# Performance work log

Measured on AMD Instinct MI355X. Metric: run time of the kernel, lower is better.

The kernel has to match this reference:

```python
import jax, jax.numpy as jnp
import numpy as np

RADII = (0.4, 0.8, 1.2)
SIGMA2 = 2.0 * 0.2 ** 2   # Gaussian shell-density bandwidth
ALPHA = 0.3               # keras LeakyReLU default
EPS = 1e-3                # keras BatchNormalization default epsilon


def _n_coeffs(L):
    return sum((2 * l + 1) ** 2 for l in range(L + 1))


def _pullback_idx(L):
    # flat index of Wigner block entry (m, n=0) for each SH coeff (l, m)
    idx, off = [], 0
    for l in range(L + 1):
        d = 2 * l + 1
        idx += [off + m * d + l for m in range(d)]
        off += d * d
    return np.asarray(idx, dtype=np.int32)


def setup_inputs() -> dict:
    key = jax.random.key(0)
    ks = jax.random.split(key, 20)
    B, N, Q, S = 64, 2048, 1024, 512
    T = [_n_coeffs(l) for l in (5, 4, 3)]  # 286, 165, 84
    f32 = jnp.float32

    def nrm(k, shape, scale=1.0):
        return jax.random.normal(ks[k], shape, dtype=f32) * scale

    dirs = nrm(1, (3, S, 3))
    dirs = dirs / jnp.linalg.norm(dirs, axis=-1, keepdims=True)
    z = lambda n: jnp.zeros((n,), f32)
    o = lambda n: jnp.ones((n,), f32)
    return {
        "x": nrm(0, (B, N, 3)),
        "shell_dirs": dirs,                                   # [3, 512, 3]
        "A_sh": nrm(2, (36, S), 1.0 / np.sqrt(S)),            # SH projection (l_max=5)
        "D_eval0": nrm(3, (Q, T[0]), 1.0 / np.sqrt(T[0])),    # Wigner eval bases
        "D_eval1": nrm(4, (Q, T[1]), 1.0 / np.sqrt(T[1])),
        "D_eval2": nrm(5, (Q, T[2]), 1.0 / np.sqrt(T[2])),
        "D_coef1": nrm(6, (T[1], Q), 1.0 / np.sqrt(Q)),       # Wigner coeff (projection) bases
        "D_coef2": nrm(7, (T[2], Q), 1.0 / np.sqrt(Q)),
        "D_coef_last": nrm(8, (T[2], Q), 1.0 / np.sqrt(Q)),
        "W0": nrm(9, (3, 16), 1.0 / np.sqrt(3)), "b0": z(16),
        "W1": nrm(10, (16, 32), 0.25), "b1": z(32),
        "W2": nrm(11, (32, 64), 1.0 / np.sqrt(32)), "b2": z(64),
        "g0": o(16), "be0": z(16),
        "g1": o(32), "be1": z(32),
        "g2": o(64), "be2": z(64),
        "Wfc1": nrm(12, (256, 512), 1.0 / 16.0), "bfc1": z(512),
        "gfc1": o(512), "befc1": z(512),
        "Wfc2": nrm(13, (512, 256), 1.0 / np.sqrt(512)), "bfc2": z(256),
        "gfc2": o(256), "befc2": z(256),
        "Wout": nrm(14, (256, 40), 1.0 / 16.0), "bout": z(40),
    }


def _bn(y, g, b, axes):
    m = jnp.mean(y, axis=axes, keepdims=True)
    v = jnp.var(y, axis=axes, keepdims=True)
    return (y - m) * jax.lax.rsqrt(v + EPS) * g + b


def reference(x, shell_dirs, A_sh, D_eval0, D_eval1, D_eval2,
              D_coef1, D_coef2, D_coef_last,
              W0, b0, W1, b1, W2, b2,
              g0, be0, g1, be1, g2, be2,
              Wfc1, bfc1, gfc1, befc1, Wfc2, bfc2, gfc2, befc2,
              Wout, bout):
    B = x.shape[0]
    # --- sphere_shell_embedding: Gaussian shell density -> SH coeffs per shell ---
    xn2 = jnp.sum(x * x, -1)[..., None]                 # [B,N,1]
    sh = []
    for i, r in enumerate(RADII):
        c = r * shell_dirs[i]                           # [S,3]
        d2 = xn2 + jnp.sum(c * c, -1) - 2.0 * (x @ c.T)  # [B,N,S]
        f = jnp.mean(jnp.exp(-d2 / SIGMA2), axis=1)      # [B,S]
        sh.append(f @ A_sh.T)                            # [B,36]
    sh = jnp.stack(sh, axis=-1)                          # [B,36,3] shells as channels
    # --- S2_to_SO3_pullback: Y_lm -> D^l_{m,0} column of Wigner blocks ---
    idx = jnp.asarray(_pullback_idx(5))
    y = jnp.zeros((B, 286, 3), sh.dtype).at[:, idx, :].set(sh)
    # --- layer 0: SO3Conv (per-coeff channel mix) + WignerEval + BN + LReLU + WignerCoeffs ---
    y = jnp.einsum('btc,cu->btu', y, W0) + b0
    y = jnp.einsum('qt,btu->bqu', D_eval0, y)            # [B,1024,16]
    y = jax.nn.leaky_relu(_bn(y, g0, be0, (0, 1)), ALPHA)
    y = jnp.einsum('tq,bqu->btu', D_coef1, y)            # [B,165,16]
    # --- layer 1 ---
    y = jnp.einsum('btc,cu->btu', y, W1) + b1
    y = jnp.einsum('qt,btu->bqu', D_eval1, y)            # [B,1024,32]
    y = jax.nn.leaky_relu(_bn(y, g1, be1, (0, 1)), ALPHA)
    y = jnp.einsum('tq,bqu->btu', D_coef2, y)            # [B,84,32]
    # --- layer 2 ---
    y = jnp.einsum('btc,cu->btu', y, W2) + b2
    y = jnp.einsum('qt,btu->bqu', D_eval2, y)            # [B,1024,64]
    y = jax.nn.leaky_relu(_bn(y, g2, be2, (0, 1)), ALPHA)
    y = jnp.einsum('tq,bqu->btu', D_coef_last, y)        # [B,84,64]
    # --- degree-wise norms (rotation-invariant pooling), l_max=3 blocks ---
    offs, sizes = (0, 1, 10, 35), (1, 9, 25, 49)
    feats = jnp.concatenate(
        [jnp.linalg.norm(y[:, o:o + s, :], axis=1, keepdims=True)
         for o, s in zip(offs, sizes)], axis=1)          # [B,4,64]
    h = feats.reshape(B, -1)                             # [B,256]
    # --- MLP head (dropout = identity at inference) ---
    h = jax.nn.relu(_bn(h @ Wfc1 + bfc1, gfc1, befc1, (0,)))
    h = jax.nn.relu(_bn(h @ Wfc2 + bfc2, gfc2, befc2, (0,)))
    return jax.nn.softmax(h @ Wout + bout, axis=-1)
```

## Files before the change

### kernel.cpp

```cpp
#include <hip/hip_runtime.h>
#include <hip/hip_bf16.h>

#define BB 64
#define NN 2048
#define QQ 1024
#define SS 512
#define NCH 16
#define PREPB 609
#define QKN3 8

__device__ const int PIDX[36] = {
    0, 2, 5, 8, 12, 17, 22, 27, 32, 38, 45, 52, 59, 66, 73, 80,
    88, 97, 106, 115, 124, 133, 142, 151, 160,
    170, 181, 192, 203, 214, 225, 236, 247, 258, 269, 280};

__global__ __launch_bounds__(256) void k_preshell(
    const float* __restrict__ De0, const float* __restrict__ De1, const float* __restrict__ De2,
    float* __restrict__ Dg0t, float* __restrict__ rs0,
    float* __restrict__ Det1, float* __restrict__ Det2,
    float* __restrict__ stats,
    const float* __restrict__ x, const float* __restrict__ dirs, float* __restrict__ pbuf) {
    __shared__ float tile[32][33];
    __shared__ float4 lx[NN / NCH];
    int blk = blockIdx.x, tid = threadIdx.x;
    if (blk < PREPB) {
        int r = tid >> 5, c = tid & 31;
        if (blk < 192) {
            int tq = blk & 31, tt = blk >> 5;
            int q0 = tq * 32, t0 = tt * 32;
            for (int rr = r; rr < 32; rr += 8) {
                int t = t0 + c;
                tile[rr][c] = (t < 165) ? De1[(q0 + rr) * 165 + t] : 0.f;
            }
            __syncthreads();
            for (int rr = r; rr < 32; rr += 8) {
                int t = t0 + rr;
                if (t < 165) Det1[t * QQ + q0 + c] = tile[c][rr];
            }
        } else if (blk < 288) {
            int i = blk - 192;
            int tq = i & 31, tt = i >> 5;
            int q0 = tq * 32, t0 = tt * 32;
            for (int rr = r; rr < 32; rr += 8) {
                int t = t0 + c;
                tile[rr][c] = (t < 84) ? De2[(q0 + rr) * 84 + t] : 0.f;
            }
            __syncthreads();
            for (int rr = r; rr < 32; rr += 8) {
                int t = t0 + rr;
                if (t < 84) Det2[t * QQ + q0 + c] = tile[c][rr];
            }
        } else if (blk < 352) {
            int i = blk - 288;
            int tq = i & 31, tj = i >> 5;
            int q0 = tq * 32, j0 = tj * 32;
            for (int rr = r; rr < 32; rr += 8) {
                int j = j0 + c;
                tile[rr][c] = (j < 36) ? De0[(q0 + rr) * 286 + PIDX[j]] : 0.f;
            }
            __syncthreads();
            for (int rr = r; rr < 32; rr += 8) {
                int j = j0 + rr;
                if (j < 36) Dg0t[j * QQ + q0 + c] = tile[c][rr];
            }
        } else if (blk < 608) {
            int w = tid >> 6, lane = tid & 63;
            int q = (blk - 352) * 4 + w;
            float s = 0.f;
#pragma unroll
            for (int p = 0; p < 5; p++) {
                int idx = lane + p * 64;
                if (idx < 286) s += De0[q * 286 + idx];
            }
#pragma unroll
            for (int o = 32; o > 0; o >>= 1) s += __shfl_xor(s, o, 64);
            if (lane == 0) rs0[q] = s;
        } else {
            if (tid < 224) stats[tid] = 0.f;
        }
        return;
    }
    int idx = blk - PREPB;
    int b = idx & 63, zc = idx >> 6;
    const float KL = 18.033688011112042f;
    const float* xb = x + ((size_t)b * NN + zc * (NN / NCH)) * 3;
    for (int n = tid; n < NN / NCH; n += 256) {
        float X = xb[n * 3 + 0];
        float Y = xb[n * 3 + 1];
        float Z = xb[n * 3 + 2];
        lx[n] = make_float4(X, Y, Z, -KL * (X * X + Y * Y + Z * Z));
    }
    __syncthreads();
    float cxs[3][2], cys[3][2], czs[3][2], bas[3][2];
#pragma unroll
    for (int i = 0; i < 3; i++) {
        float r = (i == 0) ? 0.4f : ((i == 1) ? 0.8f : 1.2f);
#pragma unroll
        for (int h = 0; h < 2; h++) {
            int s = tid + h * 256;
            float cx = r * dirs[(i * SS + s) * 3 + 0];
            float cy = r * dirs[(i * SS + s) * 3 + 1];
            float cz = r * dirs[(i * SS + s) * 3 + 2];
            bas[i][h] = -KL * (cx * cx + cy * cy + cz * cz);
            cxs[i][h] = 2.f * KL * cx;
            cys[i][h] = 2.f * KL * cy;
            czs[i][h] = 2.f * KL * cz;
        }
    }
    float acc[3][2];
#pragma unroll
    for (int i = 0; i < 3; i++) { acc[i][0] = 0.f; acc[i][1] = 0.f; }
#pragma unroll 4
    for (int n = 0; n < NN / NCH; n++) {
        float4 p = lx[n];
#pragma unroll
        for (int i = 0; i < 3; i++)
#pragma unroll
            for (int h = 0; h < 2; h++)
                acc[i][h] += __builtin_amdgcn_exp2f(
                    fmaf(cxs[i][h], p.x, fmaf(cys[i][h], p.y, fmaf(czs[i][h], p.z, p.w + bas[i][h]))));
    }
#pragma unroll
    for (int i = 0; i < 3; i++) {
        float* o = pbuf + ((size_t)(zc * 3 + i) * BB + b) * SS;
        o[tid] = acc[i][0];
        o[tid + 256] = acc[i][1];
    }
}

__global__ __launch_bounds__(256) void k_sh(const float* __restrict__ pbuf,
                                            const float* __restrict__ A_sh,
                                            float* __restrict__ lshp) {
    __shared__ float lf[256];
    int b = blockIdx.x, c = blockIdx.y, h = blockIdx.z, tid = threadIdx.x;
    float v = 0.f;
#pragma unroll
    for (int zc = 0; zc < NCH; zc++)
        v += pbuf[((size_t)(zc * 3 + c) * BB + b) * SS + h * 256 + tid];
    lf[tid] = v * (1.0f / NN);
    __syncthreads();
    int w = tid >> 6, lane = tid & 63;
    for (int j = w; j < 36; j += 4) {
        const float* As = A_sh + j * SS + h * 256;
        float a = 0.f;
#pragma unroll
        for (int k = 0; k < 4; k++) a = fmaf(lf[lane + 64 * k], As[lane + 64 * k], a);
#pragma unroll
        for (int o = 32; o > 0; o >>= 1) a += __shfl_xor(a, o, 64);
        if (lane == 0) lshp[((b * 36 + j) * 3 + c) * 2 + h] = a;
    }
}

__global__ __launch_bounds__(256) void k_eval0(const float* __restrict__ lshp,
                                               const float* __restrict__ W0,
                                               const float* __restrict__ b0,
                                               const float* __restrict__ Dg0t,
                                               const float* __restrict__ rs0,
                                               float* __restrict__ yq, float* __restrict__ stats) {
    __shared__ float lsh[36][3];
    __shared__ float llm[576];
    __shared__ float lred[4][32];
    int qc = blockIdx.x, b = blockIdx.y, tid = threadIdx.x;
    if (tid < 108) {
        int j = tid / 3, c = tid % 3;
        lsh[j][c] = lshp[((b * 36 + j) * 3 + c) * 2 + 0] + lshp[((b * 36 + j) * 3 + c) * 2 + 1];
    }
    __syncthreads();
    for (int i = tid; i < 576; i += 256) {
        int j = i >> 4, u = i & 15;
        float m = 0.f;
#pragma unroll
        for (int c = 0; c < 3; c++) m = fmaf(lsh[j][c], W0[c * 16 + u], m);
        llm[i] = m;
    }
    __syncthreads();
    int q = qc * 256 + tid;
    float acc[16];
#pragma unroll
    for (int u = 0; u < 16; u++) acc[u] = 0.f;
#pragma unroll 4
    for (int j = 0; j < 36; j++) {
        float d = Dg0t[j * QQ + q];
#pragma unroll
        for (int u = 0; u < 16; u++) acc[u] = fmaf(d, llm[j * 16 + u], acc[u]);
    }
    float rb = rs0[q];
#pragma unroll
    for (int u = 0; u < 16; u++) acc[u] = fmaf(b0[u], rb, acc[u]);
#pragma unroll
    for (int u = 0; u < 16; u++) yq[((size_t)b * 16 + u) * QQ + q] = acc[u];
    int lane = tid & 63, w = tid >> 6;
#pragma unroll
    for (int u = 0; u < 16; u++) {
        float v = acc[u], v2 = acc[u] * acc[u];
#pragma unroll
        for (int o = 32; o > 0; o >>= 1) {
            v += __shfl_xor(v, o, 64);
            v2 += __shfl_xor(v2, o, 64);
        }
        if (lane == 0) { lred[w][u] = v; lred[w][16 + u] = v2; }
    }
    __syncthreads();
    if (tid < 32) atomicAdd(&stats[tid], lred[0][tid] + lred[1][tid] + lred[2][tid] + lred[3][tid]);
}

template <int TT, int UU, int QKN>
__global__ __launch_bounds__(256) void k_coefG(const float* __restrict__ yq,
                                               const float* __restrict__ Dc,
                                               const float* __restrict__ stats,
                                               const float* __restrict__ g,
                                               const float* __restrict__ be,
                                               float* __restrict__ part) {
    constexpr int KC = QQ / QKN;
    __shared__ float lA[32][68];
    __shared__ float lB[32][68];
    __shared__ float lsu[UU], ltu[UU];
    int mt = blockIdx.x, nt = blockIdx.y, qk = blockIdx.z, tid = threadIdx.x;
    int m0 = mt * 64, n0 = nt * 64, k0 = qk * KC;
    if (tid < UU) {
        const float inv = 1.0f / (BB * QQ);
        float mm = stats[tid] * inv;
        float var = stats[UU + tid] * inv - mm * mm;
        float s = g[tid] * rsqrtf(fmaxf(var, 0.f) + 1e-3f);
        lsu[tid] = s;
        ltu[tid] = be[tid] - mm * s;
    }
    __syncthreads();
    int r = tid >> 2, f = (tid & 3) * 4;
    bool mok = (m0 + r) < TT;
    const float* arow = Dc + (size_t)(mok ? (m0 + r) : 0) * QQ;
    const float* brow = yq + (size_t)(n0 + r) * QQ;
    float su = lsu[(n0 + r) % UU], tu = ltu[(n0 + r) % UU];
    int tg = tid >> 4, ug = tid & 15;
    float acc[4][4];
#pragma unroll
    for (int i = 0; i < 4; i++)
#pragma unroll
        for (int j = 0; j < 4; j++) acc[i][j] = 0.f;
    for (int kb = 0; kb < KC; kb += 32) {
        int kg = k0 + kb;
#pragma unroll
        for (int p = 0; p < 2; p++) {
            int ko = f + p * 16;
            float4 a4 = make_float4(0.f, 0.f, 0.f, 0.f);
            if (mok) a4 = *(const float4*)(arow + kg + ko);
            float4 b4 = *(const float4*)(brow + kg + ko);
#pragma unroll
            for (int i = 0; i < 4; i++) {
                float v = fmaf((&b4.x)[i], su, tu);
                lA[ko + i][r] = (&a4.x)[i];
                lB[ko + i][r] = (v > 0.f) ? v : 0.3f * v;
            }
        }
        __syncthreads();
#pragma unroll 2
        for (int kk = 0; kk < 32; kk++) {
            float4 a4 = *(const float4*)&lA[kk][tg * 4];
            float4 b4 = *(const float4*)&lB[kk][ug * 4];
#pragma unroll
            for (int i = 0; i < 4; i++) {
                float av = (&a4.x)[i];
                acc[i][0] = fmaf(av, b4.x, acc[i][0]);
                acc[i][1] = fmaf(av, b4.y, acc[i][1]);
                acc[i][2] = fmaf(av, b4.z, acc[i][2]);
                acc[i][3] = fmaf(av, b4.w, acc[i][3]);
            }
        }
        __syncthreads();
    }
    int n = n0 + ug * 4;
    int b = n / UU, u0 = n % UU;
#pragma unroll
    for (int i = 0; i < 4; i++) {
        int t = m0 + tg * 4 + i;
        if (t < TT)
            *(float4*)&part[(((size_t)qk * BB + b) * TT + t) * UU + u0] =
                make_float4(acc[i][0], acc[i][1], acc[i][2], acc[i][3]);
    }
}

template <int TT, int CC, int UU, int QKN, int TTp, int TS>
__global__ __launch_bounds__(256) void k_redmix(const float* __restrict__ part,
                                                const float* __restrict__ W,
                                                const float* __restrict__ bias,
                                                float* __restrict__ ym) {
    constexpr int TSL = TTp / TS;
    __shared__ float lyt[TSL][CC + 1];
    int b = blockIdx.x, ts = blockIdx.y, tid = threadIdx.x;
    int t0 = ts * TSL;
    for (int i = tid; i < TSL * CC; i += 256) {
        int tl = i / CC, c = i % CC;
        int t = t0 + tl;
        float v = 0.f;
        if (t < TT) {
#pragma unroll
            for (int k = 0; k < QKN; k++)
                v += part[(size_t)k * (BB * TT * CC) + ((size_t)b * TT + t) * CC + c];
        }
        lyt[tl][c] = v;
    }
    __syncthreads();
    for (int i = tid; i < UU * TSL; i += 256) {
        int u = i / TSL, tl = i % TSL;
        int t = t0 + tl;
        float m = 0.f;
        if (t < TT) {
            m = bias[u];
#pragma unroll
            for (int c = 0; c < CC; c++) m = fmaf(lyt[tl][c], W[c * UU + u], m);
        }
        ym[((size_t)b * UU + u) * TTp + t] = m;
    }
}

template <int TT, int TTp, int UU>
__global__ __launch_bounds__(256) void k_evalG(const float* __restrict__ ym,
                                               const float* __restrict__ Det,
                                               float* __restrict__ yq,
                                               float* __restrict__ stats) {
    __shared__ float lA[32][68];
    __shared__ float lB[32][68];
    __shared__ float sred[2][64];
    int mt = blockIdx.x, qt = blockIdx.y, tid = threadIdx.x;
    int m0 = mt * 64, q0 = qt * 64;
    int r = tid >> 2, f = (tid & 3) * 4;
    const float* arow = ym + (size_t)(m0 + r) * TTp;
    int br = tid >> 4, bq = (tid & 15) * 4;
    int tg = tid >> 4, ug = tid & 15;
    float acc[4][4];
#pragma unroll
    for (int i = 0; i < 4; i++)
#pragma unroll
        for (int j = 0; j < 4; j++) acc[i][j] = 0.f;
    for (int kb = 0; kb < TT; kb += 32) {
#pragma unroll
        for (int p = 0; p < 2; p++) {
            int ko = f + p * 16;
            float4 a4 = *(const float4*)(arow + kb + ko);
#pragma unroll
            for (int i = 0; i < 4; i++) lA[ko + i][r] = (&a4.x)[i];
            int kk = br + p * 16;
            int t = kb + kk;
            float4 b4 = make_float4(0.f, 0.f, 0.f, 0.f);
            if (t < TT) b4 = *(const float4*)(Det + (size_t)t * QQ + q0 + bq);
            *(float4*)&lB[kk][bq] = b4;
        }
        __syncthreads();
#pragma unroll 2
        for (int kk = 0; kk < 32; kk++) {
            float4 a4 = *(const float4*)&lA[kk][tg * 4];
            float4 b4 = *(const float4*)&lB[kk][ug * 4];
#pragma unroll
            for (int i = 0; i < 4; i++) {
                float av = (&a4.x)[i];
                acc[i][0] = fmaf(av, b4.x, acc[i][0]);
                acc[i][1] = fmaf(av, b4.y, acc[i][1]);
                acc[i][2] = fmaf(av, b4.z, acc[i][2]);
                acc[i][3] = fmaf(av, b4.w, acc[i][3]);
            }
        }
        __syncthreads();
    }
    float s1[4], s2[4];
#pragma unroll
    for (int i = 0; i < 4; i++) {
        int m = m0 + tg * 4 + i;
        *(float4*)&yq[(size_t)m * QQ + q0 + ug * 4] =
            make_float4(acc[i][0], acc[i][1], acc[i][2], acc[i][3]);
        s1[i] = (acc[i][0] + acc[i][1]) + (acc[i][2] + acc[i][3]);
        s2[i] = fmaf(acc[i][0], acc[i][0], fmaf(acc[i][1], acc[i][1],
                 fmaf(acc[i][2], acc[i][2], acc[i][3] * acc[i][3])));
    }
#pragma unroll
    for (int o = 1; o < 16; o <<= 1) {
#pragma unroll
        for (int i = 0; i < 4; i++) {
            s1[i] += __shfl_xor(s1[i], o, 64);
            s2[i] += __shfl_xor(s2[i], o, 64);
        }
    }
    if (ug == 0) {
#pragma unroll
        for (int i = 0; i < 4; i++) {
            sred[0][tg * 4 + i] = s1[i];
            sred[1][tg * 4 + i] = s2[i];
        }
    }
    __syncthreads();
    if (tid < 2 * UU) {
        int which = tid / UU, u = tid % UU;
        float s = 0.f;
        for (int rr = u; rr < 64; rr += UU) s += sred[which][rr];
        atomicAdd(&stats[which * UU + u], s);
    }
}

__global__ __launch_bounds__(256) void k_norms(const float* __restrict__ part, float* __restrict__ ht0) {
    __shared__ float red[4][64];
    int b = blockIdx.x, blk = blockIdx.y;
    int tq = threadIdx.x >> 6, u = threadIdx.x & 63;
    const int offs[4] = {0, 1, 10, 35};
    const int ends[4] = {1, 10, 35, 84};
    float a = 0.f;
    for (int t = offs[blk] + tq; t < ends[blk]; t += 4) {
        float v = 0.f;
#pragma unroll
        for (int k = 0; k < QKN3; k++)
            v += part[(size_t)k * (BB * 84 * 64) + (b * 84 + t) * 64 + u];
        a = fmaf(v, v, a);
    }
    red[tq][u] = a;
    __syncthreads();
    if (tq == 0) {
        float s = red[0][u] + red[1][u] + red[2][u] + red[3][u];
        ht0[(blk * 64 + u) * BB + b] = sqrtf(fmaxf(s, 0.f));
    }
}

template <int K, int J>
__global__ __launch_bounds__(512) void k_fc(const float* __restrict__ in, const float* __restrict__ W,
                                            const float* __restrict__ bias, const float* __restrict__ g,
                                            const float* __restrict__ be, float* __restrict__ out) {
    __shared__ float red[8][64];
    int j = blockIdx.x;
    int b = threadIdx.x & 63, kq = threadIdx.x >> 6;
    constexpr int KS = K / 8;
    int kbeg = kq * KS;
    float a0 = 0.f, a1 = 0.f, a2 = 0.f, a3 = 0.f;
#pragma unroll 4
    for (int k = kbeg; k < kbeg + KS; k += 4) {
        a0 = fmaf(in[k * BB + b], W[(size_t)k * J + j], a0);
        a1 = fmaf(in[(k + 1) * BB + b], W[(size_t)(k + 1) * J + j], a1);
        a2 = fmaf(in[(k + 2) * BB + b], W[(size_t)(k + 2) * J + j], a2);
        a3 = fmaf(in[(k + 3) * BB + b], W[(size_t)(k + 3) * J + j], a3);
    }
    red[kq][b] = (a0 + a1) + (a2 + a3);
    __syncthreads();
    if (kq == 0) {
        float acc = bias[j];
#pragma unroll
        for (int i = 0; i < 8; i++) acc += red[i][b];
        float s1 = acc, s2 = acc * acc;
#pragma unroll
        for (int o = 32; o > 0; o >>= 1) {
            s1 += __shfl_xor(s1, o, 64);
            s2 += __shfl_xor(s2, o, 64);
        }
        float m = s1 * (1.0f / 64.f);
        float var = s2 * (1.0f / 64.f) - m * m;
        float sc = g[j] * rsqrtf(fmaxf(var, 0.f) + 1e-3f);
        float v = (acc - m) * sc + be[j];
        out[j * BB + b] = fmaxf(v, 0.f);
    }
}

__global__ __launch_bounds__(256) void k_out(const float* __restrict__ ht2, const float* __restrict__ Wout,
                                             const float* __restrict__ bout, float* __restrict__ outp) {
    __shared__ float red[4][64];
    __shared__ float sm[64];
    int b = blockIdx.x;
    int o = threadIdx.x & 63, kq = threadIdx.x >> 6;
    float a0 = 0.f, a1 = 0.f, a2 = 0.f, a3 = 0.f;
    int kbeg = kq * 64;
    if (o < 40) {
#pragma unroll 4
        for (int k = kbeg; k < kbeg + 64; k += 4) {
            a0 = fmaf(ht2[k * BB + b], Wout[k * 40 + o], a0);
            a1 = fmaf(ht2[(k + 1) * BB + b], Wout[(k + 1) * 40 + o], a1);
            a2 = fmaf(ht2[(k + 2) * BB + b], Wout[(k + 2) * 40 + o], a2);
            a3 = fmaf(ht2[(k + 3) * BB + b], Wout[(k + 3) * 40 + o], a3);
        }
    }
    red[kq][o] = (a0 + a1) + (a2 + a3);
    __syncthreads();
    if (kq == 0) {
        float acc = red[0][o] + red[1][o] + red[2][o] + red[3][o] + ((o < 40) ? bout[o] : 0.f);
        sm[o] = (o < 40) ? acc : -3.0e38f;
        __syncthreads();
        for (int s = 32; s > 0; s >>= 1) {
            if (o < s) sm[o] = fmaxf(sm[o], sm[o + s]);
            __syncthreads();
        }
        float m = sm[0];
        __syncthreads();
        const float L2E = 1.4426950408889634f;
        float e = (o < 40) ? exp2f((acc - m) * L2E) : 0.f;
        sm[o] = e;
        __syncthreads();
        for (int s = 32; s > 0; s >>= 1) {
            if (o < s) sm[o] += sm[o + s];
            __syncthreads();
        }
        if (o < 40) outp[b * 40 + o] = e / sm[0];
    }
}

#define OFF_PBUF 0
#define OFF_DG0T 1572864
#define OFF_RS0 1609728
#define OFF_DET1 1610752
#define OFF_DET2 1779712
#define OFF_YQ 1865728
#define OFF_YM 6060032
#define OFF_LSH 6453248
#define OFF_HT0 6467072
#define OFF_HT1 6483456
#define OFF_HT2 6516224
#define OFF_STATS 6532608
#define OFF_PART 6532864
#define OFF_PART3 7909120

extern "C" void kernel_launch(void* const* d_in, const int* in_sizes, int n_in,
                              void* d_out, int out_size, void* d_ws, size_t ws_size,
                              hipStream_t stream) {
    const float* x = (const float*)d_in[0];
    const float* shell_dirs = (const float*)d_in[1];
    const float* A_sh = (const float*)d_in[2];
    const float* D_eval0 = (const float*)d_in[3];
    const float* D_eval1 = (const float*)d_in[4];
    const float* D_eval2 = (const float*)d_in[5];
    const float* D_coef1 = (const float*)d_in[6];
    const float* D_coef2 = (const float*)d_in[7];
    const float* D_coef_last = (const float*)d_in[8];
    const float* W0 = (const float*)d_in[9];
    const float* b0 = (const float*)d_in[10];
    const float* W1 = (const float*)d_in[11];
    const float* b1 = (const float*)d_in[12];
    const float* W2 = (const float*)d_in[13];
    const float* b2 = (const float*)d_in[14];
    const float* g0 = (const float*)d_in[15];
    const float* be0 = (const float*)d_in[16];
    const float* g1 = (const float*)d_in[17];
    const float* be1 = (const float*)d_in[18];
    const float* g2 = (const float*)d_in[19];
    const float* be2 = (const float*)d_in[20];
    const float* Wfc1 = (const float*)d_in[21];
    const float* bfc1 = (const float*)d_in[22];
    const float* gfc1 = (const float*)d_in[23];
    const float* befc1 = (const float*)d_in[24];
    const float* Wfc2 = (const float*)d_in[25];
    const float* bfc2 = (const float*)d_in[26];
    const float* gfc2 = (const float*)d_in[27];
    const float* befc2 = (const float*)d_in[28];
    const float* Wout = (const float*)d_in[29];
    const float* bout = (const float*)d_in[30];
    float* out = (float*)d_out;

    float* ws = (float*)d_ws;
    float* pbuf = ws + OFF_PBUF;
    float* Dg0t = ws + OFF_DG0T;
    float* rs0 = ws + OFF_RS0;
    float* Det1 = ws + OFF_DET1;
    float* Det2 = ws + OFF_DET2;
    float* yq = ws + OFF_YQ;
    float* ym = ws + OFF_YM;
    float* lshp = ws + OFF_LSH;
    float* ht0 = ws + OFF_HT0;
    float* ht1 = ws + OFF_HT1;
    float* ht2 = ws + OFF_HT2;
    float* stats = ws + OFF_STATS;
    float* part = ws + OFF_PART;
    float* part3 = ws + OFF_PART3;
    float* stats0 = stats;
    float* stats1 = stats + 32;
    float* stats2 = stats + 96;

    k_preshell<<<PREPB + BB * NCH, 256, 0, stream>>>(
        D_eval0, D_eval1, D_eval2, Dg0t, rs0, Det1, Det2, stats, x, shell_dirs, pbuf);
    k_sh<<<dim3(BB, 3, 2), 256, 0, stream>>>(pbuf, A_sh, lshp);
    k_eval0<<<dim3(4, BB), 256, 0, stream>>>(lshp, W0, b0, Dg0t, rs0, yq, stats0);
    k_coefG<165, 16, 8><<<dim3(3, 16, 8), 256, 0, stream>>>(yq, D_coef1, stats0, g0, be0, part);
    k_redmix<165, 16, 32, 8, 192, 8><<<dim3(BB, 8), 256, 0, stream>>>(part, W1, b1, ym);
    k_evalG<165, 192, 32><<<dim3(32, 16), 256, 0, stream>>>(ym, Det1, yq, stats1);
    k_coefG<84, 32, 8><<<dim3(2, 32, 8), 256, 0, stream>>>(yq, D_coef2, stats1, g1, be1, part);
    k_redmix<84, 32, 64, 8, 96, 8><<<dim3(BB, 8), 256, 0, stream>>>(part, W2, b2, ym);
    k_evalG<84, 96, 64><<<dim3(64, 16), 256, 0, stream>>>(ym, Det2, yq, stats2);
    k_coefG<84, 64, QKN3><<<dim3(2, 64, QKN3), 256, 0, stream>>>(yq, D_coef_last, stats2, g2, be2, part3);
    k_norms<<<dim3(BB, 4), 256, 0, stream>>>(part3, ht0);
    k_fc<256, 512><<<512, 512, 0, stream>>>(ht0, Wfc1, bfc1, gfc1, befc1, ht1);
    k_fc<512, 256><<<256, 512, 0, stream>>>(ht1, Wfc2, bfc2, gfc2, befc2, ht2);
    k_out<<<BB, 256, 0, stream>>>(ht2, Wout, bout, out);
}
```

Baseline: 312.5 us.

## Fuse channel mixing into coef GEMM epilogue and defer split-K reduction to eval

Removes the separate k_redmix kernels. Each split-K slice of the coefficient GEMM now applies the channel-mixing weights in its epilogue and writes a partial mixed result, adding the bias only in slice 0. The eval GEMM sums the eight partial slices while loading its A operand. This saves two launches and a round trip through the partial buffer, at the cost of redundant mixing work per slice and eight times the A-operand reads in k_evalG.

```diff
diff --git a/kernel.cpp b/kernel.cpp
--- a/kernel.cpp
+++ b/kernel.cpp
@@ -8,6 +8,7 @@
 #define NCH 16
 #define PREPB 609
 #define QKN3 8
+#define YMSZ (BB * 32 * 192)
 
 __device__ const int PIDX[36] = {
     0, 2, 5, 8, 12, 17, 22, 27, 32, 38, 45, 52, 59, 66, 73, 80,
@@ -202,6 +203,97 @@
     }
     __syncthreads();
     if (tid < 32) atomicAdd(&stats[tid], lred[0][tid] + lred[1][tid] + lred[2][tid] + lred[3][tid]);
+}
+
+template <int TT, int UU, int QKN, int UU2, int TTp>
+__global__ __launch_bounds__(256) void k_coefM(const float* __restrict__ yq,
+                                               const float* __restrict__ Dc,
+                                               const float* __restrict__ stats,
+                                               const float* __restrict__ g,
+                                               const float* __restrict__ be,
+                                               const float* __restrict__ Wn,
+                                               const float* __restrict__ bn,
+                                               float* __restrict__ ymp) {
+    constexpr int KC = QQ / QKN;
+    constexpr int NB = 64 / UU;
+    __shared__ __align__(16) float sm[4352];
+    __shared__ float lsu[UU], ltu[UU];
+    float* lA = sm;
+    float* lB = sm + 2176;
+    float* lC = sm;
+    int mt = blockIdx.x, nt = blockIdx.y, qk = blockIdx.z, tid = threadIdx.x;
+    int m0 = mt * 64, n0 = nt * 64, k0 = qk * KC;
+    if (tid < UU) {
+        const float inv = 1.0f / (BB * QQ);
+        float mm = stats[tid] * inv;
+        float var = stats[UU + tid] * inv - mm * mm;
+        float s = g[tid] * rsqrtf(fmaxf(var, 0.f) + 1e-3f);
+        lsu[tid] = s;
+        ltu[tid] = be[tid] - mm * s;
+    }
+    __syncthreads();
+    int r = tid >> 2, f = (tid & 3) * 4;
+    bool mok = (m0 + r) < TT;
+    const float* arow = Dc + (size_t)(mok ? (m0 + r) : 0) * QQ;
+    const float* brow = yq + (size_t)(n0 + r) * QQ;
+    float su = lsu[(n0 + r) % UU], tu = ltu[(n0 + r) % UU];
+    int tg = tid >> 4, ug = tid & 15;
+    float acc[4][4];
+#pragma unroll
+    for (int i = 0; i < 4; i++)
+#pragma unroll
+        for (int j = 0; j < 4; j++) acc[i][j] = 0.f;
+    for (int kb = 0; kb < KC; kb += 32) {
+        int kg = k0 + kb;
+#pragma unroll
+        for (int p = 0; p < 2; p++) {
+            int ko = f + p * 16;
+            float4 a4 = make_float4(0.f, 0.f, 0.f, 0.f);
+            if (mok) a4 = *(const float4*)(arow + kg + ko);
+            float4 b4 = *(const float4*)(brow + kg + ko);
+#pragma unroll
+            for (int i = 0; i < 4; i++) {
+                float v = fmaf((&b4.x)[i], su, tu);
+                lA[(ko + i) * 68 + r] = (&a4.x)[i];
+                lB[(ko + i) * 68 + r] = (v > 0.f) ? v : 0.3f * v;
+            }
+        }
+        __syncthreads();
+#pragma unroll 2
+        for (int kk = 0; kk < 32; kk++) {
+            float4 a4 = *(const float4*)&lA[kk * 68 + tg * 4];
+            float4 b4 = *(const float4*)&lB[kk * 68 + ug * 4];
+#pragma unroll
+            for (int i = 0; i < 4; i++) {
+                float av = (&a4.x)[i];
+                acc[i][0] = fmaf(av, b4.x, acc[i][0]);
+                acc[i][1] = fmaf(av, b4.y, acc[i][1]);
+                acc[i][2] = fmaf(av, b4.z, acc[i][2]);
+                acc[i][3] = fmaf(av, b4.w, acc[i][3]);
+            }
+        }
+        __syncthreads();
+    }
+#pragma unroll
+    for (int i = 0; i < 4; i++)
+#pragma unroll
+        for (int j = 0; j < 4; j++)
+            lC[(tg * 4 + i) * 65 + ug * 4 + j] = acc[i][j];
+    __syncthreads();
+    for (int i = tid; i < 64 * NB * UU2; i += 256) {
+        int tl = i & 63;
+        int rest = i >> 6;
+        int b_l = rest % NB;
+        int u2 = rest / NB;
+        int tglob = m0 + tl;
+        if (tglob >= TTp) continue;
+        float val = (qk == 0 && tglob < TT) ? bn[u2] : 0.f;
+#pragma unroll
+        for (int c = 0; c < UU; c++)
+            val = fmaf(lC[tl * 65 + b_l * UU + c], Wn[c * UU2 + u2], val);
+        int bg = n0 / UU + b_l;
+        ymp[(size_t)qk * YMSZ + ((size_t)bg * UU2 + u2) * TTp + tglob] = val;
+    }
 }
 
 template <int TT, int UU, int QKN>
@@ -279,42 +371,8 @@
     }
 }
 
-template <int TT, int CC, int UU, int QKN, int TTp, int TS>
-__global__ __launch_bounds__(256) void k_redmix(const float* __restrict__ part,
-                                                const float* __restrict__ W,
-                                                const float* __restrict__ bias,
-                                                float* __restrict__ ym) {
-    constexpr int TSL = TTp / TS;
-    __shared__ float lyt[TSL][CC + 1];
-    int b = blockIdx.x, ts = blockIdx.y, tid = threadIdx.x;
-    int t0 = ts * TSL;
-    for (int i = tid; i < TSL * CC; i += 256) {
-        int tl = i / CC, c = i % CC;
-        int t = t0 + tl;
-        float v = 0.f;
-        if (t < TT) {
-#pragma unroll
-            for (int k = 0; k < QKN; k++)
-                v += part[(size_t)k * (BB * TT * CC) + ((size_t)b * TT + t) * CC + c];
-        }
-        lyt[tl][c] = v;
-    }
-    __syncthreads();
-    for (int i = tid; i < UU * TSL; i += 256) {
-        int u = i / TSL, tl = i % TSL;
-        int t = t0 + tl;
-        float m = 0.f;
-        if (t < TT) {
-            m = bias[u];
-#pragma unroll
-            for (int c = 0; c < CC; c++) m = fmaf(lyt[tl][c], W[c * UU + u], m);
-        }
-        ym[((size_t)b * UU + u) * TTp + t] = m;
-    }
-}
-
-template <int TT, int TTp, int UU>
-__global__ __launch_bounds__(256) void k_evalG(const float* __restrict__ ym,
+template <int TT, int TTp, int UU, int QKN>
+__global__ __launch_bounds__(256) void k_evalG(const float* __restrict__ ymp,
                                                const float* __restrict__ Det,
                                                float* __restrict__ yq,
                                                float* __restrict__ stats) {
@@ -324,7 +382,7 @@
     int mt = blockIdx.x, qt = blockIdx.y, tid = threadIdx.x;
     int m0 = mt * 64, q0 = qt * 64;
     int r = tid >> 2, f = (tid & 3) * 4;
-    const float* arow = ym + (size_t)(m0 + r) * TTp;
+    const float* arow = ymp + (size_t)(m0 + r) * TTp;
     int br = tid >> 4, bq = (tid & 15) * 4;
     int tg = tid >> 4, ug = tid & 15;
     float acc[4][4];
@@ -336,7 +394,12 @@
 #pragma unroll
         for (int p = 0; p < 2; p++) {
             int ko = f + p * 16;
-            float4 a4 = *(const float4*)(arow + kb + ko);
+            float4 a4 = make_float4(0.f, 0.f, 0.f, 0.f);
+#pragma unroll
+            for (int k = 0; k < QKN; k++) {
+                float4 v = *(const float4*)(arow + (size_t)k * YMSZ + kb + ko);
+                a4.x += v.x; a4.y += v.y; a4.z += v.z; a4.w += v.w;
+            }
 #pragma unroll
             for (int i = 0; i < 4; i++) lA[ko + i][r] = (&a4.x)[i];
             int kk = br + p * 16;
@@ -501,14 +564,13 @@
 #define OFF_DET1 1610752
 #define OFF_DET2 1779712
 #define OFF_YQ 1865728
-#define OFF_YM 6060032
-#define OFF_LSH 6453248
-#define OFF_HT0 6467072
-#define OFF_HT1 6483456
-#define OFF_HT2 6516224
-#define OFF_STATS 6532608
-#define OFF_PART 6532864
-#define OFF_PART3 7909120
+#define OFF_YMP 6060032
+#define OFF_LSH 9205760
+#define OFF_HT0 9219584
+#define OFF_HT1 9235968
+#define OFF_HT2 9268736
+#define OFF_STATS 9285120
+#define OFF_PART3 9285376
 
 extern "C" void kernel_launch(void* const* d_in, const int* in_sizes, int n_in,
                               void* d_out, int out_size, void* d_ws, size_t ws_size,
@@ -553,13 +615,12 @@
     float* Det1 = ws + OFF_DET1;
     float* Det2 = ws + OFF_DET2;
     float* yq = ws + OFF_YQ;
-    float* ym = ws + OFF_YM;
+    float* ymp = ws + OFF_YMP;
     float* lshp = ws + OFF_LSH;
     float* ht0 = ws + OFF_HT0;
     float* ht1 = ws + OFF_HT1;
     float* ht2 = ws + OFF_HT2;
     float* stats = ws + OFF_STATS;
-    float* part = ws + OFF_PART;
     float* part3 = ws + OFF_PART3;
     float* stats0 = stats;
     float* stats1 = stats + 32;
@@ -569,12 +630,12 @@
         D_eval0, D_eval1, D_eval2, Dg0t, rs0, Det1, Det2, stats, x, shell_dirs, pbuf);
     k_sh<<<dim3(BB, 3, 2), 256, 0, stream>>>(pbuf, A_sh, lshp);
     k_eval0<<<dim3(4, BB), 256, 0, stream>>>(lshp, W0, b0, Dg0t, rs0, yq, stats0);
-    k_coefG<165, 16, 8><<<dim3(3, 16, 8), 256, 0, stream>>>(yq, D_coef1, stats0, g0, be0, part);
-    k_redmix<165, 16, 32, 8, 192, 8><<<dim3(BB, 8), 256, 0, stream>>>(part, W1, b1, ym);
-    k_evalG<165, 192, 32><<<dim3(32, 16), 256, 0, stream>>>(ym, Det1, yq, stats1);
-    k_coefG<84, 32, 8><<<dim3(2, 32, 8), 256, 0, stream>>>(yq, D_coef2, stats1, g1, be1, part);
-    k_redmix<84, 32, 64, 8, 96, 8><<<dim3(BB, 8), 256, 0, stream>>>(part, W2, b2, ym);
-    k_evalG<84, 96, 64><<<dim3(64, 16), 256, 0, stream>>>(ym, Det2, yq, stats2);
+    k_coefM<165, 16, 8, 32, 192><<<dim3(3, 16, 8), 256, 0, stream>>>(
+        yq, D_coef1, stats0, g0, be0, W1, b1, ymp);
+    k_evalG<165, 192, 32, 8><<<dim3(32, 16), 256, 0, stream>>>(ymp, Det1, yq, stats1);
+    k_coefM<84, 32, 8, 64, 96><<<dim3(2, 32, 8), 256, 0, stream>>>(
+        yq, D_coef2, stats1, g1, be1, W2, b2, ymp);
+    k_evalG<84, 96, 64, 8><<<dim3(64, 16), 256, 0, stream>>>(ymp, Det2, yq, stats2);
     k_coefG<84, 64, QKN3><<<dim3(2, 64, QKN3), 256, 0, stream>>>(yq, D_coef_last, stats2, g2, be2, part3);
     k_norms<<<dim3(BB, 4), 256, 0, stream>>>(part3, ht0);
     k_fc<256, 512><<<512, 512, 0, stream>>>(ht0, Wfc1, bfc1, gfc1, befc1, ht1);
```

Measured after the change: 345.0 us. 10.4% more time.
